# Kernel tuning notes

Measured on AMD Instinct MI355X. Metric: run time of the kernel, lower is better.

Reference implementation:

```python
import jax, jax.numpy as jnp
import numpy as np

N, T = 4, 2048
FEAT, VEC = 512, 16          # feat_size, vec_size
K = 8192                     # codebook_size = prediction_encoder.output_size
CIN = 512                    # prediction_encoder.input_size
OFFSET = 0
IGNORE = -100                # torch CrossEntropyLoss default ignore_index
EPS = 1e-12                  # torch F.normalize eps


def setup_inputs() -> dict:
    key = jax.random.key(0)
    k1, k2, k3, k4, k5, k6 = jax.random.split(key, 6)
    feats = jax.random.normal(k1, (N, T, FEAT), dtype=jnp.float32)
    context = jax.random.normal(k2, (N, T, CIN), dtype=jnp.float32)
    lens = jax.random.randint(k3, (N,), T // 2, T + 1, dtype=jnp.int32)
    # xavier_normal_ for (feat_size, vec_size)
    proj_matrix = jax.random.normal(k4, (FEAT, VEC), dtype=jnp.float32) * np.sqrt(2.0 / (FEAT + VEC))
    cb = jax.random.normal(k5, (K, VEC), dtype=jnp.float32)
    codebook = cb / jnp.maximum(jnp.linalg.norm(cb, axis=1, keepdims=True), EPS)
    W_enc = jax.random.normal(k6, (CIN, K), dtype=jnp.float32) / np.sqrt(CIN)
    b_enc = jnp.zeros((K,), dtype=jnp.float32)
    return {"feats": feats, "context": context, "lens": lens,
            "proj_matrix": proj_matrix, "codebook": codebook,
            "W_enc": W_enc, "b_enc": b_enc}


def reference(feats, context, lens, proj_matrix, codebook, W_enc, b_enc):
    # prediction encoder: Linear(CIN -> K), lens unchanged
    logits = jnp.einsum("ntc,ck->ntk", context, W_enc) + b_enc      # (N,T,K)

    # --- target computation (no_grad in torch) ---
    f = feats[:, OFFSET:] @ proj_matrix                              # (N,T',V)
    f = f / jnp.maximum(jnp.linalg.norm(f, axis=-1, keepdims=True), EPS)
    # squared distance ||f - c||^2 = |f|^2 - 2 f.c + |c|^2; argmin equals
    # argmin of vector_norm since sqrt is monotone. Avoids (N,T,K,V) tensor.
    d2 = (jnp.sum(f * f, axis=-1, keepdims=True)
          - 2.0 * jnp.einsum("ntv,kv->ntk", f, codebook)
          + jnp.sum(codebook * codebook, axis=-1))                   # (N,T',K)
    targets = jnp.argmin(d2, axis=2).astype(jnp.int32)               # (N,T')
    Tp = T - OFFSET
    mask = (lens[:, None] - OFFSET) > jnp.arange(Tp)[None, :]        # (N,T')
    targets = jnp.where(mask, targets, IGNORE)

    # --- masked cross entropy (mean over non-ignored) ---
    logits_f = logits[:, OFFSET:].reshape(-1, K)                     # (N*T',K)
    targets_f = targets.reshape(-1)
    logp = jax.nn.log_softmax(logits_f, axis=-1)
    valid = targets_f != IGNORE
    safe_t = jnp.where(valid, targets_f, 0)
    nll = -jnp.take_along_axis(logp, safe_t[:, None], axis=1)[:, 0]
    loss = jnp.sum(nll * valid) / jnp.maximum(jnp.sum(valid), 1)
    return loss
```

## Files before the change

### kernel.cpp

```cpp
#include <hip/hip_runtime.h>
#include <hip/hip_bf16.h>
#include <hip/hip_fp8.h>

#define MROWS 8192
#define KDIM  512
#define NCOL  8192
#define TSEQ  2048

typedef float f32x4 __attribute__((ext_vector_type(4)));

__device__ __forceinline__ unsigned int pack4_fp8(float a, float b, float c, float d) {
#if __has_builtin(__builtin_amdgcn_cvt_pk_fp8_f32)
  int r = __builtin_amdgcn_cvt_pk_fp8_f32(a, b, 0, false);
  r = __builtin_amdgcn_cvt_pk_fp8_f32(c, d, r, true);
  return (unsigned int)r;
#else
  __hip_fp8_e4m3 ha(a), hb(b), hc(c), hd(d);
  return (unsigned int)ha.__x | ((unsigned int)hb.__x << 8) |
         ((unsigned int)hc.__x << 16) | ((unsigned int)hd.__x << 24);
#endif
}

__device__ __forceinline__ float fp8d(unsigned char b) {
  unsigned int s = b >> 7, e = (b >> 3) & 15, m = b & 7;
  if (e == 0) {
    float v = (float)m * 0.001953125f;
    return s ? -v : v;
  }
  unsigned int bits = (s << 31) | ((e + 120) << 23) | (m << 20);
  return __uint_as_float(bits);
}

__global__ void prep_kernel(const float* __restrict__ X, unsigned char* __restrict__ A8,
                            const float* __restrict__ W, unsigned char* __restrict__ B8,
                            const float* __restrict__ feats, const float* __restrict__ proj,
                            float* __restrict__ F, unsigned long long* __restrict__ amin,
                            float* __restrict__ rowsum) {
  __shared__ float tile[64][65];
  const int tid = threadIdx.x;
  int b = blockIdx.x;
  if (b < 4096) {
    int i = b * 256 + tid;
    float4 v = reinterpret_cast<const float4*>(X)[i];
    reinterpret_cast<unsigned int*>(A8)[i] = pack4_fp8(v.x, v.y, v.z, v.w);
  } else if (b < 5120) {
    b -= 4096;
    const int bx = b & 127, by = b >> 7;
    const int c4 = tid & 15, rr = tid >> 4;
    #pragma unroll
    for (int p = 0; p < 4; ++p) {
      int row = p * 16 + rr;
      float4 v = reinterpret_cast<const float4*>(W + (size_t)(by * 64 + row) * NCOL + bx * 64)[c4];
      tile[row][c4 * 4 + 0] = v.x; tile[row][c4 * 4 + 1] = v.y;
      tile[row][c4 * 4 + 2] = v.z; tile[row][c4 * 4 + 3] = v.w;
    }
    __syncthreads();
    #pragma unroll
    for (int p = 0; p < 4; ++p) {
      int oc = p * 16 + rr;
      unsigned int pk = pack4_fp8(tile[c4 * 4 + 0][oc], tile[c4 * 4 + 1][oc],
                                  tile[c4 * 4 + 2][oc], tile[c4 * 4 + 3][oc]);
      *reinterpret_cast<unsigned int*>(B8 + (size_t)(bx * 64 + oc) * KDIM + by * 64 + c4 * 4) = pk;
    }
  } else if (b < 5632) {
    b -= 5120;
    int rl = tid >> 4, d = tid & 15;
    int row = b * 16 + rl;
    const float4* fr4 = reinterpret_cast<const float4*>(feats + (size_t)row * KDIM);
    float acc = 0.f;
    #pragma unroll 4
    for (int kc = 0; kc < KDIM / 4; ++kc) {
      float4 v = fr4[kc];
      const float* p = proj + (size_t)kc * 64 + d;
      acc += v.x * p[0] + v.y * p[16] + v.z * p[32] + v.w * p[48];
    }
    F[(size_t)row * 16 + d] = acc;
  } else {
    int r = (b - 5632) * 256 + tid;
    amin[r] = ~0ull;
    rowsum[r] = 0.f;
  }
}

#define GEMM_BLOCKS 4096
#define CB_CODES 128

__device__ __forceinline__ void gld16(const void* g, void* l3) {
  __builtin_amdgcn_global_load_lds((const __attribute__((address_space(1))) void*)g,
                                   (__attribute__((address_space(3))) void*)l3, 16, 0, 0);
}

__global__ __launch_bounds__(256, 4)
void gemm_targets_kernel(const unsigned char* __restrict__ A,
                         const unsigned char* __restrict__ B,
                         const float* __restrict__ bias,
                         float* __restrict__ rowsum,
                         const float* __restrict__ F,
                         const float* __restrict__ cb,
                         unsigned long long* __restrict__ amin) {
  __shared__ __align__(16) unsigned char smem[32768];
  const int tid = threadIdx.x;
  const int bid = blockIdx.x;

  if (bid >= GEMM_BLOCKS) {
    float (*csh)[16] = (float (*)[16])smem;
    const int tb = bid - GEMM_BLOCKS;
    const int r0 = (tb & 7) * 1024 + tid;
    const int c0 = (tb >> 3) * CB_CODES;
    {
      int ci = tid >> 1, half = tid & 1;
      const float4* src = reinterpret_cast<const float4*>(cb + (size_t)(c0 + ci) * 16 + half * 8);
      float4 v0 = src[0], v1 = src[1];
      float4* dst = reinterpret_cast<float4*>(&csh[ci][half * 8]);
      dst[0] = v0; dst[1] = v1;
    }
    float4 fa[4][4];
    #pragma unroll
    for (int q = 0; q < 4; ++q) {
      const float4* fp = reinterpret_cast<const float4*>(F + (size_t)(r0 + q * 256) * 16);
      fa[q][0] = fp[0]; fa[q][1] = fp[1]; fa[q][2] = fp[2]; fa[q][3] = fp[3];
    }
    __syncthreads();

    float best[4] = {3.4e38f, 3.4e38f, 3.4e38f, 3.4e38f};
    int bidx[4] = {0, 0, 0, 0};
    #pragma unroll 2
    for (int ci = 0; ci < CB_CODES; ++ci) {
      const float4* cvp = reinterpret_cast<const float4*>(&csh[ci][0]);
      float4 c0v = cvp[0], c1v = cvp[1], c2v = cvp[2], c3v = cvp[3];
      #pragma unroll
      for (int q = 0; q < 4; ++q) {
        float dot = fa[q][0].x*c0v.x + fa[q][0].y*c0v.y + fa[q][0].z*c0v.z + fa[q][0].w*c0v.w
                  + fa[q][1].x*c1v.x + fa[q][1].y*c1v.y + fa[q][1].z*c1v.z + fa[q][1].w*c1v.w
                  + fa[q][2].x*c2v.x + fa[q][2].y*c2v.y + fa[q][2].z*c2v.z + fa[q][2].w*c2v.w
                  + fa[q][3].x*c3v.x + fa[q][3].y*c3v.y + fa[q][3].z*c3v.z + fa[q][3].w*c3v.w;
        float d = -dot;
        if (d < best[q]) { best[q] = d; bidx[q] = c0 + ci; }
      }
    }
    #pragma unroll
    for (int q = 0; q < 4; ++q) {
      unsigned int u = __float_as_uint(best[q]);
      unsigned int key = (u & 0x80000000u) ? ~u : (u | 0x80000000u);
      unsigned long long pk = ((unsigned long long)key << 32) | (unsigned int)bidx[q];
      atomicMin(&amin[r0 + q * 256], pk);
    }
    return;
  }

  const int wave = tid >> 6;
  const int lane = tid & 63;
  const int xcd = bid & 7, idx = bid >> 3;
  const int bx = xcd * 8 + (idx & 7);
  const int by = idx >> 3;
  const int row0 = by * 128;
  const int col0 = bx * 128;
  const int wr = wave >> 1, wc = wave & 1;
  unsigned char* As = smem;
  unsigned char* Bs = smem + 16384;

  f32x4 acc[4][4];
  #pragma unroll
  for (int i = 0; i < 4; ++i)
    #pragma unroll
    for (int j = 0; j < 4; ++j) acc[i][j] = (f32x4){0.f, 0.f, 0.f, 0.f};

  const int lr = lane >> 2;
  const int lcs = (((lane & 3) ^ ((lane >> 3) & 3)) << 4);

  const int l15 = lane & 15, l16 = lane >> 4;
  const int sw = (l15 >> 1) & 3;
  const int subo = (l16 & 1) * 8;
  const int lg16 = l16 >> 1;

  for (int kt = 0; kt < KDIM; kt += 128) {
    #pragma unroll
    for (int c = 0; c < 2; ++c) {
      int rchunk = (wave * 2 + c) * 16;
      #pragma unroll
      for (int kp = 0; kp < 2; ++kp) {
        gld16(A + (size_t)(row0 + rchunk + lr) * KDIM + kt + kp * 64 + lcs,
              As + kp * 8192 + rchunk * 64);
        gld16(B + (size_t)(col0 + rchunk + lr) * KDIM + kt + kp * 64 + lcs,
              Bs + kp * 8192 + rchunk * 64);
      }
    }
    __syncthreads();
    #pragma unroll
    for (int ks = 0; ks < 4; ++ks) {
      const int kpl = (ks >> 1) * 8192;
      const int poff = ((((ks & 1) * 2 + lg16) ^ sw) << 4) + subo;
      long af[4], bb[4];
      #pragma unroll
      for (int mi = 0; mi < 4; ++mi)
        af[mi] = *(const long*)(As + kpl + (wr * 64 + mi * 16 + l15) * 64 + poff);
      #pragma unroll
      for (int ni = 0; ni < 4; ++ni)
        bb[ni] = *(const long*)(Bs + kpl + (wc * 64 + ni * 16 + l15) * 64 + poff);
      #pragma unroll
      for (int mi = 0; mi < 4; ++mi)
        #pragma unroll
        for (int ni = 0; ni < 4; ++ni)
          acc[mi][ni] = __builtin_amdgcn_mfma_f32_16x16x32_fp8_fp8(af[mi], bb[ni], acc[mi][ni], 0, 0, 0);
    }
    __syncthreads();
  }

  float bv[4];
  #pragma unroll
  for (int ni = 0; ni < 4; ++ni)
    bv[ni] = bias[col0 + wc * 64 + ni * 16 + l15];
  #pragma unroll
  for (int mi = 0; mi < 4; ++mi) {
    int rbase = row0 + wr * 64 + mi * 16 + l16 * 4;
    #pragma unroll
    for (int j = 0; j < 4; ++j) {
      float se = 0.f;
      #pragma unroll
      for (int ni = 0; ni < 4; ++ni)
        se += __expf(acc[mi][ni][j] + bv[ni]);
      #pragma unroll
      for (int o = 1; o < 16; o <<= 1) se += __shfl_xor(se, o);
      if (l15 == 0) atomicAdd(&rowsum[rbase + j], se);
    }
  }
}

__global__ void tgt_logit_kernel(const unsigned char* __restrict__ A,
                                 const unsigned char* __restrict__ B,
                                 const float* __restrict__ bias,
                                 const unsigned long long* __restrict__ amin,
                                 float* __restrict__ tgtlog) {
  const int wv = threadIdx.x >> 6, lane = threadIdx.x & 63;
  const int r = blockIdx.x * 4 + wv;
  const int tg = (int)(amin[r] & 0xffffffffull);
  uint2 ua = reinterpret_cast<const uint2*>(A + (size_t)r * KDIM)[lane];
  uint2 ub = reinterpret_cast<const uint2*>(B + (size_t)tg * KDIM)[lane];
  float s = 0.f;
  const unsigned char* pa = reinterpret_cast<const unsigned char*>(&ua);
  const unsigned char* pb = reinterpret_cast<const unsigned char*>(&ub);
  #pragma unroll
  for (int i = 0; i < 8; ++i) s += fp8d(pa[i]) * fp8d(pb[i]);
  #pragma unroll
  for (int o = 1; o < 64; o <<= 1) s += __shfl_xor(s, o);
  if (lane == 0) tgtlog[r] = s + bias[tg];
}

__global__ void loss_kernel(const float* __restrict__ rowsum, const float* __restrict__ tgtl,
                            const int* __restrict__ lens, float* __restrict__ out) {
  __shared__ float sh[256];
  __shared__ int shc[256];
  int tid = threadIdx.x;
  float s = 0.f; int c = 0;
  for (int r = tid; r < MROWS; r += 256) {
    int n = r >> 11;
    int t = r & (TSEQ - 1);
    if (t < lens[n]) { s += logf(rowsum[r]) - tgtl[r]; c++; }
  }
  sh[tid] = s; shc[tid] = c;
  __syncthreads();
  for (int o = 128; o > 0; o >>= 1) {
    if (tid < o) { sh[tid] += sh[tid + o]; shc[tid] += shc[tid + o]; }
    __syncthreads();
  }
  if (tid == 0) out[0] = sh[0] / (float)max(shc[0], 1);
}

extern "C" void kernel_launch(void* const* d_in, const int* in_sizes, int n_in,
                              void* d_out, int out_size, void* d_ws, size_t ws_size,
                              hipStream_t stream) {
  const float* feats    = (const float*)d_in[0];
  const float* context  = (const float*)d_in[1];
  const int*   lens     = (const int*)d_in[2];
  const float* proj     = (const float*)d_in[3];
  const float* codebook = (const float*)d_in[4];
  const float* W_enc    = (const float*)d_in[5];
  const float* b_enc    = (const float*)d_in[6];
  float* out = (float*)d_out;

  char* ws = (char*)d_ws;
  unsigned char* A8 = (unsigned char*)(ws);
  unsigned char* B8 = (unsigned char*)(ws + 4194304);
  float* F          = (float*)(ws + 8388608);
  unsigned long long* amin = (unsigned long long*)(ws + 8912896);
  float* rowsum     = (float*)(ws + 8978432);
  float* tgtlog     = (float*)(ws + 9011200);

  prep_kernel<<<5664, 256, 0, stream>>>(context, A8, W_enc, B8, feats, proj, F, amin, rowsum);
  gemm_targets_kernel<<<GEMM_BLOCKS + 512, 256, 0, stream>>>(A8, B8, b_enc, rowsum, F, codebook, amin);
  tgt_logit_kernel<<<MROWS / 4, 256, 0, stream>>>(A8, B8, b_enc, amin, tgtlog);
  loss_kernel<<<1, 256, 0, stream>>>(rowsum, tgtlog, lens, out);
}
```

Before: 196.5 us.

## Halve GEMM K-tile to 64 and schedule target-search blocks first

The fused GEMM kernel's K-step shrinks from 128 to 64 bytes, cutting shared memory per block from 32KB to 16KB, which may let more blocks fit on each CU. The argmin codebook-search blocks now come first in the grid instead of after the GEMM blocks, so their work overlaps with the GEMM rather than trailing as a tail. The cost is twice as many barrier-separated load/compute iterations with less work per sync, and no double buffering.

```diff
diff --git a/kernel.cpp b/kernel.cpp
--- a/kernel.cpp
+++ b/kernel.cpp
@@ -82,7 +82,7 @@
   }
 }
 
-#define GEMM_BLOCKS 4096
+#define TGT_BLOCKS 512
 #define CB_CODES 128
 
 __device__ __forceinline__ void gld16(const void* g, void* l3) {
@@ -98,15 +98,14 @@
                          const float* __restrict__ F,
                          const float* __restrict__ cb,
                          unsigned long long* __restrict__ amin) {
-  __shared__ __align__(16) unsigned char smem[32768];
+  __shared__ __align__(16) unsigned char smem[16384];
   const int tid = threadIdx.x;
   const int bid = blockIdx.x;
 
-  if (bid >= GEMM_BLOCKS) {
+  if (bid < TGT_BLOCKS) {
     float (*csh)[16] = (float (*)[16])smem;
-    const int tb = bid - GEMM_BLOCKS;
-    const int r0 = (tb & 7) * 1024 + tid;
-    const int c0 = (tb >> 3) * CB_CODES;
+    const int r0 = (bid & 7) * 1024 + tid;
+    const int c0 = (bid >> 3) * CB_CODES;
     {
       int ci = tid >> 1, half = tid & 1;
       const float4* src = reinterpret_cast<const float4*>(cb + (size_t)(c0 + ci) * 16 + half * 8);
@@ -148,16 +147,17 @@
     return;
   }
 
+  const int gid = bid - TGT_BLOCKS;
   const int wave = tid >> 6;
   const int lane = tid & 63;
-  const int xcd = bid & 7, idx = bid >> 3;
+  const int xcd = gid & 7, idx = gid >> 3;
   const int bx = xcd * 8 + (idx & 7);
   const int by = idx >> 3;
   const int row0 = by * 128;
   const int col0 = bx * 128;
   const int wr = wave >> 1, wc = wave & 1;
   unsigned char* As = smem;
-  unsigned char* Bs = smem + 16384;
+  unsigned char* Bs = smem + 8192;
 
   f32x4 acc[4][4];
   #pragma unroll
@@ -173,30 +173,24 @@
   const int subo = (l16 & 1) * 8;
   const int lg16 = l16 >> 1;
 
-  for (int kt = 0; kt < KDIM; kt += 128) {
+  for (int kt = 0; kt < KDIM; kt += 64) {
     #pragma unroll
     for (int c = 0; c < 2; ++c) {
       int rchunk = (wave * 2 + c) * 16;
-      #pragma unroll
-      for (int kp = 0; kp < 2; ++kp) {
-        gld16(A + (size_t)(row0 + rchunk + lr) * KDIM + kt + kp * 64 + lcs,
-              As + kp * 8192 + rchunk * 64);
-        gld16(B + (size_t)(col0 + rchunk + lr) * KDIM + kt + kp * 64 + lcs,
-              Bs + kp * 8192 + rchunk * 64);
-      }
-    }
-    __syncthreads();
-    #pragma unroll
-    for (int ks = 0; ks < 4; ++ks) {
-      const int kpl = (ks >> 1) * 8192;
-      const int poff = ((((ks & 1) * 2 + lg16) ^ sw) << 4) + subo;
+      gld16(A + (size_t)(row0 + rchunk + lr) * KDIM + kt + lcs, As + rchunk * 64);
+      gld16(B + (size_t)(col0 + rchunk + lr) * KDIM + kt + lcs, Bs + rchunk * 64);
+    }
+    __syncthreads();
+    #pragma unroll
+    for (int ks = 0; ks < 2; ++ks) {
+      const int poff = (((ks * 2 + lg16) ^ sw) << 4) + subo;
       long af[4], bb[4];
       #pragma unroll
       for (int mi = 0; mi < 4; ++mi)
-        af[mi] = *(const long*)(As + kpl + (wr * 64 + mi * 16 + l15) * 64 + poff);
+        af[mi] = *(const long*)(As + (wr * 64 + mi * 16 + l15) * 64 + poff);
       #pragma unroll
       for (int ni = 0; ni < 4; ++ni)
-        bb[ni] = *(const long*)(Bs + kpl + (wc * 64 + ni * 16 + l15) * 64 + poff);
+        bb[ni] = *(const long*)(Bs + (wc * 64 + ni * 16 + l15) * 64 + poff);
       #pragma unroll
       for (int mi = 0; mi < 4; ++mi)
         #pragma unroll
@@ -287,7 +281,7 @@
   float* tgtlog     = (float*)(ws + 9011200);
 
   prep_kernel<<<5664, 256, 0, stream>>>(context, A8, W_enc, B8, feats, proj, F, amin, rowsum);
-  gemm_targets_kernel<<<GEMM_BLOCKS + 512, 256, 0, stream>>>(A8, B8, b_enc, rowsum, F, codebook, amin);
+  gemm_targets_kernel<<<TGT_BLOCKS + 4096, 256, 0, stream>>>(A8, B8, b_enc, rowsum, F, codebook, amin);
   tgt_logit_kernel<<<MROWS / 4, 256, 0, stream>>>(A8, B8, b_enc, amin, tgtlog);
   loss_kernel<<<1, 256, 0, stream>>>(rowsum, tgtlog, lens, out);
 }
```

Measured after the change: 190.7 us. 1.03x faster.
